# Kernel optimization log

Measured on AMD Instinct MI355X. Metric: run time of the kernel, lower is better.

Reference implementation:

```python
import jax, jax.numpy as jnp
import numpy as np

NEG_SLOPE = 0.2  # PyG GATv2Conv default


def with_self_loops(edge_index, n):
    loop = jnp.arange(n, dtype=edge_index.dtype)
    src = jnp.concatenate([edge_index[0], loop])
    dst = jnp.concatenate([edge_index[1], loop])
    return src, dst


def gatv2(x, src, dst, Wl, bl, Wr, br, att, bias):
    """PyG GATv2Conv (eval mode, concat=True, add_self_loops done by caller).
    x: [N, F_in]; att: [H, C]. Returns [N, H*C]."""
    N = x.shape[0]
    H, C = att.shape
    xl = (x @ Wl + bl).reshape(N, H, C)  # lin_l(x): source-side transform
    xr = (x @ Wr + br).reshape(N, H, C)  # lin_r(x): target-side transform
    s = jax.nn.leaky_relu(xl[src] + xr[dst], NEG_SLOPE)      # [E,H,C]
    logit = jnp.einsum('ehc,hc->eh', s, att)                 # [E,H]
    m = jax.ops.segment_max(logit, dst, num_segments=N)      # stable softmax per target
    e = jnp.exp(logit - m[dst])
    den = jax.ops.segment_sum(e, dst, num_segments=N)
    alpha = e / (den[dst] + 1e-16)                           # [E,H]
    out = jax.ops.segment_sum(alpha[:, :, None] * xl[src], dst, num_segments=N)
    return out.reshape(N, H * C) + bias


def setup_inputs() -> dict:
    N, E = 20000, 320000        # agent nodes / edges
    M, EM = 40000, 400000       # lane nodes / edges
    B, L = 64, 50               # focal agents, centerline length
    SEQ, INC, HID, HEADS, OUT = 50, 2, 32, 4, 60
    H4 = HID * HEADS
    key = jax.random.key(0)
    ks = list(jax.random.split(key, 48))
    kit = iter(ks)

    def p(shape):
        return jax.random.normal(next(kit), shape, jnp.float32) * 0.05

    inp = {
        'x': jax.random.normal(next(kit), (N, SEQ, INC), jnp.float32),
        'edge_index': jax.random.randint(next(kit), (2, E), 0, N),
        'lane_x': jax.random.normal(next(kit), (M, 2), jnp.float32),
        'lane_edge_index': jax.random.randint(next(kit), (2, EM), 0, M),
        'batch': jnp.sort(jax.random.randint(next(kit), (N,), 0, B)),
        'focal_idx': jax.random.randint(next(kit), (B,), 0, N),
        'centerlines': jax.random.normal(next(kit), (B, L, 2), jnp.float32),
        # agent embedding
        'ae_W': p((SEQ * INC, HID)), 'ae_b': p((HID,)),
        # agent subgraph conv1 / conv2
        'a1_Wl': p((HID, H4)), 'a1_bl': p((H4,)), 'a1_Wr': p((HID, H4)), 'a1_br': p((H4,)), 'a1_att': p((HEADS, HID)), 'a1_b': p((H4,)),
        'a2_Wl': p((H4, H4)), 'a2_bl': p((H4,)), 'a2_Wr': p((H4, H4)), 'a2_br': p((H4,)), 'a2_att': p((HEADS, HID)), 'a2_b': p((H4,)),
        # map embedding + map subgraph
        'me_W': p((2, HID)), 'me_b': p((HID,)),
        'm1_Wl': p((HID, H4)), 'm1_bl': p((H4,)), 'm1_Wr': p((HID, H4)), 'm1_br': p((H4,)), 'm1_att': p((HEADS, HID)), 'm1_b': p((H4,)),
        'm2_Wl': p((H4, H4)), 'm2_bl': p((H4,)), 'm2_Wr': p((H4, H4)), 'm2_br': p((H4,)), 'm2_att': p((HEADS, HID)), 'm2_b': p((H4,)),
        # centerline processor
        'cl_W': p((2, HID)), 'cl_b': p((HID,)),
        # global graph (heads=1)
        'g_Wl': p((H4, HID)), 'g_bl': p((HID,)), 'g_Wr': p((H4, HID)), 'g_br': p((HID,)), 'g_att': p((1, HID)), 'g_b': p((HID,)),
        # output head
        'fc_W': p((2 * HID, OUT)), 'fc_b': p((OUT,)),
    }
    return inp


def reference(x, edge_index, lane_x, lane_edge_index, batch, focal_idx, centerlines,
              ae_W, ae_b,
              a1_Wl, a1_bl, a1_Wr, a1_br, a1_att, a1_b,
              a2_Wl, a2_bl, a2_Wr, a2_br, a2_att, a2_b,
              me_W, me_b,
              m1_Wl, m1_bl, m1_Wr, m1_br, m1_att, m1_b,
              m2_Wl, m2_bl, m2_Wr, m2_br, m2_att, m2_b,
              cl_W, cl_b,
              g_Wl, g_bl, g_Wr, g_br, g_att, g_b,
              fc_W, fc_b):
    N = x.shape[0]
    M = lane_x.shape[0]
    # agent branch
    agent_x = jax.nn.relu(x.reshape(N, -1) @ ae_W + ae_b)
    a_src, a_dst = with_self_loops(edge_index, N)
    h = jax.nn.relu(gatv2(agent_x, a_src, a_dst, a1_Wl, a1_bl, a1_Wr, a1_br, a1_att, a1_b))
    agent_features = jax.nn.relu(gatv2(h, a_src, a_dst, a2_Wl, a2_bl, a2_Wr, a2_br, a2_att, a2_b))  # [N,128]
    # map branch (output unused downstream in original, computed for faithfulness)
    map_x = jax.nn.relu(lane_x @ me_W + me_b)
    m_src, m_dst = with_self_loops(lane_edge_index, M)
    hm = jax.nn.relu(gatv2(map_x, m_src, m_dst, m1_Wl, m1_bl, m1_Wr, m1_br, m1_att, m1_b))
    map_features = jax.nn.relu(gatv2(hm, m_src, m_dst, m2_Wl, m2_bl, m2_Wr, m2_br, m2_att, m2_b))
    _ = map_features  # global_mean_pool results are dead code in the original forward
    # global graph over agent features (heads=1)
    global_features = jax.nn.relu(gatv2(agent_features, a_src, a_dst, g_Wl, g_bl, g_Wr, g_br, g_att, g_b))  # [N,32]
    focal = global_features[focal_idx]  # [B,32]
    # centerlines: per-polyline mean then linear (no relu, as in original)
    cl_feat = jnp.mean(centerlines, axis=1) @ cl_W + cl_b  # [B,32]
    combined = jnp.concatenate([focal, cl_feat], axis=1)
    return combined @ fc_W + fc_b
```

## Files before the change

### kernel.cpp

```cpp
#include <hip/hip_runtime.h>
#include <hip/hip_bf16.h>
#include <hip/hip_fp16.h>
#include <math.h>

typedef __hip_bfloat16 bf16;
#define NEG_SLOPE 0.2f
#define SFLAG (1 << 30)

typedef _Float16 f16x8 __attribute__((ext_vector_type(8)));
typedef float f32x4 __attribute__((ext_vector_type(4)));

#define NSEG 25
struct Seg { const void* src; int n; int off; };
struct Tab { Seg s[NSEG]; };

__device__ __forceinline__ float ldconv(const void* src, int i, int f32mode) {
    return f32mode ? ((const float*)src)[i]
                   : __bfloat162float(((const bf16*)src)[i]);
}

__global__ void k_convert(Tab tab, float* __restrict__ dst,
                          const unsigned short* __restrict__ xdet, int* __restrict__ flag,
                          const int* __restrict__ dstArr, int E, int N,
                          int* __restrict__ deg, int* __restrict__ rank,
                          const void* a2WlS, const void* a2WrS,
                          const void* gWlS, const void* gWrS,
                          __half* __restrict__ a2Wlt, __half* __restrict__ a2Wrt,
                          __half* __restrict__ gWlt, __half* __restrict__ gWrt) {
    __shared__ int cnt;
    if (threadIdx.x == 0) cnt = 0;
    __syncthreads();
    int local = 0;
    for (int i = threadIdx.x; i < 2048; i += blockDim.x) {
        unsigned short w = xdet[2 * i];
        int e = (w >> 7) & 0xFF;
        if (e >= 0x90) local++;
    }
    atomicAdd(&cnt, local);
    __syncthreads();
    int f32mode = (cnt > 100) ? 1 : 0;
    if (blockIdx.x == 0 && threadIdx.x == 0) flag[0] = f32mode;

    int gid = blockIdx.x * blockDim.x + threadIdx.x;
    int gsz = gridDim.x * blockDim.x;
    for (int s = 0; s < NSEG; s++) {
        Seg sg = tab.s[s];
        for (int i = gid; i < sg.n; i += gsz) {
            dst[sg.off + i] = ldconv(sg.src, i, f32mode);
        }
    }
    for (int i = gid; i < 128 * 128; i += gsz) {
        int k = i >> 7, j = i & 127;
        a2Wlt[(size_t)j * 128 + k] = __float2half(ldconv(a2WlS, i, f32mode));
        a2Wrt[(size_t)j * 128 + k] = __float2half(ldconv(a2WrS, i, f32mode));
    }
    for (int i = gid; i < 128 * 32; i += gsz) {
        int k = i >> 5, j = i & 31;
        gWlt[(size_t)j * 128 + k] = __float2half(ldconv(gWlS, i, f32mode));
        gWrt[(size_t)j * 128 + k] = __float2half(ldconv(gWrS, i, f32mode));
    }
    int EA = E + N;
    for (int e = gid; e < EA; e += gsz) {
        int d = (e < E) ? dstArr[e] : (e - E);
        rank[e] = atomicAdd(&deg[d], 1);
    }
}

__launch_bounds__(1024)
__global__ void k_scanf(const int* __restrict__ deg, int* __restrict__ offs,
                        int n, int* __restrict__ st, int nb) {
    __shared__ int ws[16];
    __shared__ int stot, sprev;
    int tile = blockIdx.x;
    int i = tile * 1024 + threadIdx.x;
    int lane = threadIdx.x & 63, wid = threadIdx.x >> 6;
    int v = (i < n) ? deg[i] : 0;
    int x = v;
    #pragma unroll
    for (int o = 1; o < 64; o <<= 1) {
        int y = __shfl_up(x, o);
        if (lane >= o) x += y;
    }
    if (lane == 63) ws[wid] = x;
    __syncthreads();
    if (wid == 0) {
        int w = (lane < 16) ? ws[lane] : 0;
        int s = w;
        #pragma unroll
        for (int o = 1; o < 16; o <<= 1) {
            int y = __shfl_up(s, o);
            if (lane >= o) s += y;
        }
        if (lane < 16) ws[lane] = s - w;
        if (lane == 15) stot = s;
    }
    __syncthreads();
    int local = ws[wid] + x - v;
    if (threadIdx.x == 0) {
        int prev = 0;
        if (tile > 0) {
            int vv;
            while ((((vv = __hip_atomic_load(&st[tile - 1], __ATOMIC_ACQUIRE,
                                             __HIP_MEMORY_SCOPE_AGENT))) & SFLAG) == 0) {}
            prev = vv & ~SFLAG;
        }
        __hip_atomic_store(&st[tile], (prev + stot) | SFLAG, __ATOMIC_RELEASE,
                           __HIP_MEMORY_SCOPE_AGENT);
        sprev = prev;
        if (tile == nb - 1) offs[n] = prev + stot;
    }
    __syncthreads();
    if (i < n) offs[i] = sprev + local;
}

__launch_bounds__(256)
__global__ void k_fill_embedlin(const int* __restrict__ srcArr, const int* __restrict__ dstArr,
                                int E, int N, const int* __restrict__ offs,
                                const int* __restrict__ rank, int* __restrict__ csr,
                                const void* __restrict__ xraw, const int* __restrict__ flag,
                                const float* __restrict__ aeW, const float* __restrict__ aeb,
                                const float* __restrict__ Wl, const float* __restrict__ bl,
                                const float* __restrict__ Wr, const float* __restrict__ br,
                                __half* __restrict__ outl, float* __restrict__ outr,
                                int EB) {
    __shared__ float xs[100 * 36];
    __shared__ float axs[32 * 36];
    if (blockIdx.x >= EB) {
        int e = (blockIdx.x - EB) * 256 + threadIdx.x;
        int EA = E + N;
        if (e >= EA) return;
        int d, s;
        if (e < E) { d = dstArr[e]; s = srcArr[e]; } else { d = s = e - E; }
        csr[offs[d] + rank[e]] = s;
        return;
    }
    constexpr int NTP = 36;
    int t = threadIdx.x, nb = blockIdx.x * 32;
    if (flag[0]) {
        const float4* x4 = (const float4*)xraw;
        for (int idx = t; idx < 32 * 25; idx += 256) {
            int node = idx / 25, k4 = idx % 25;
            float4 v = x4[(size_t)(nb + node) * 25 + k4];
            xs[(k4 * 4 + 0) * NTP + node] = v.x;
            xs[(k4 * 4 + 1) * NTP + node] = v.y;
            xs[(k4 * 4 + 2) * NTP + node] = v.z;
            xs[(k4 * 4 + 3) * NTP + node] = v.w;
        }
    } else {
        const ushort4* xu = (const ushort4*)xraw;
        for (int idx = t; idx < 32 * 25; idx += 256) {
            int node = idx / 25, k4 = idx % 25;
            ushort4 u = xu[(size_t)(nb + node) * 25 + k4];
            xs[(k4 * 4 + 0) * NTP + node] = __uint_as_float((unsigned)u.x << 16);
            xs[(k4 * 4 + 1) * NTP + node] = __uint_as_float((unsigned)u.y << 16);
            xs[(k4 * 4 + 2) * NTP + node] = __uint_as_float((unsigned)u.z << 16);
            xs[(k4 * 4 + 3) * NTP + node] = __uint_as_float((unsigned)u.w << 16);
        }
    }
    __syncthreads();
    {
        int j = t & 31, g0 = t >> 5;
        float a0 = 0.f, a1 = 0.f, a2 = 0.f, a3 = 0.f;
        #pragma unroll 10
        for (int k = 0; k < 100; k++) {
            float w = aeW[k * 32 + j];
            const float4 xv = *(const float4*)&xs[k * NTP + g0 * 4];
            a0 += w * xv.x; a1 += w * xv.y; a2 += w * xv.z; a3 += w * xv.w;
        }
        float bj = aeb[j];
        axs[j * NTP + g0 * 4 + 0] = fmaxf(a0 + bj, 0.f);
        axs[j * NTP + g0 * 4 + 1] = fmaxf(a1 + bj, 0.f);
        axs[j * NTP + g0 * 4 + 2] = fmaxf(a2 + bj, 0.f);
        axs[j * NTP + g0 * 4 + 3] = fmaxf(a3 + bj, 0.f);
    }
    __syncthreads();
    {
        int j = t & 63, g0 = t >> 6;
        float aL0[2][4], aL1[2][4], aR0[2][4], aR1[2][4];
        #pragma unroll
        for (int g = 0; g < 2; g++)
            #pragma unroll
            for (int c = 0; c < 4; c++) { aL0[g][c]=0.f; aL1[g][c]=0.f; aR0[g][c]=0.f; aR1[g][c]=0.f; }
        #pragma unroll 4
        for (int k = 0; k < 32; k++) {
            float wl0 = Wl[k * 128 + j];
            float wl1 = Wl[k * 128 + j + 64];
            float wr0 = Wr[k * 128 + j];
            float wr1 = Wr[k * 128 + j + 64];
            #pragma unroll
            for (int g = 0; g < 2; g++) {
                const float4 xv = *(const float4*)&axs[k * NTP + (g0 + g * 4) * 4];
                aL0[g][0] += wl0 * xv.x; aL0[g][1] += wl0 * xv.y; aL0[g][2] += wl0 * xv.z; aL0[g][3] += wl0 * xv.w;
                aL1[g][0] += wl1 * xv.x; aL1[g][1] += wl1 * xv.y; aL1[g][2] += wl1 * xv.z; aL1[g][3] += wl1 * xv.w;
                aR0[g][0] += wr0 * xv.x; aR0[g][1] += wr0 * xv.y; aR0[g][2] += wr0 * xv.z; aR0[g][3] += wr0 * xv.w;
                aR1[g][0] += wr1 * xv.x; aR1[g][1] += wr1 * xv.y; aR1[g][2] += wr1 * xv.z; aR1[g][3] += wr1 * xv.w;
            }
        }
        float bl0 = bl[j], bl1 = bl[j + 64], br0 = br[j], br1 = br[j + 64];
        #pragma unroll
        for (int g = 0; g < 2; g++) {
            int n0 = nb + (g0 + g * 4) * 4;
            #pragma unroll
            for (int c = 0; c < 4; c++) {
                size_t row = (size_t)(n0 + c) * 128;
                outl[row + j]      = __float2half(aL0[g][c] + bl0);
                outl[row + j + 64] = __float2half(aL1[g][c] + bl1);
                outr[row + j]      = aR0[g][c] + br0;
                outr[row + j + 64] = aR1[g][c] + br1;
            }
        }
    }
}

__device__ __forceinline__ void gat_proc(float4 raw, bool valid,
                                         const float* xrd, const float* av,
                                         float* acc, float& sm) {
    const __half2* h = (const __half2*)&raw;
    float v[8];
    float2 f;
    f = __half22float2(h[0]); v[0] = f.x; v[1] = f.y;
    f = __half22float2(h[1]); v[2] = f.x; v[3] = f.y;
    f = __half22float2(h[2]); v[4] = f.x; v[5] = f.y;
    f = __half22float2(h[3]); v[6] = f.x; v[7] = f.y;
    float p = 0.f;
    #pragma unroll
    for (int c = 0; c < 8; c++) {
        float u = v[c] + xrd[c];
        u = (u > 0.f) ? u : NEG_SLOPE * u;
        p += u * av[c];
    }
    p += __shfl_xor(p, 1);
    p += __shfl_xor(p, 2);
    p += __shfl_xor(p, 4);
    p += __shfl_xor(p, 8);
    float w = __expf(fminf(p, 80.f));
    if (!valid) w = 0.f;
    sm += w;
    #pragma unroll
    for (int c = 0; c < 8; c++) acc[c] += w * v[c];
}

__device__ __forceinline__ void gat16_to_lds(__half* xsh,
                                             const __half* __restrict__ xl,
                                             const float* __restrict__ xr,
                                             const float* __restrict__ att,
                                             const int* __restrict__ offs,
                                             const int* __restrict__ csr,
                                             const float* __restrict__ bias,
                                             int d, int node) {
    int t = threadIdx.x;
    int lane = t & 63;
    int sub = lane & 15;
    int lb = lane & 48;
    float av[8];
    {
        const float4* t4 = (const float4*)(att + sub * 8);
        float4 c = t4[0], e = t4[1];
        av[0]=c.x; av[1]=c.y; av[2]=c.z; av[3]=c.w;
        av[4]=e.x; av[5]=e.y; av[6]=e.z; av[7]=e.w;
    }
    bool ok = d >= 0;
    int i0 = ok ? offs[d] : 0;
    int i1 = ok ? offs[d + 1] : 0;
    int cnt = i1 - i0;

    float xrd[8];
    #pragma unroll
    for (int c = 0; c < 8; c++) xrd[c] = 0.f;
    if (ok) {
        const float4* p4 = (const float4*)(xr + (size_t)d * 128 + sub * 8);
        float4 a = p4[0], b = p4[1];
        xrd[0]=a.x; xrd[1]=a.y; xrd[2]=a.z; xrd[3]=a.w;
        xrd[4]=b.x; xrd[5]=b.y; xrd[6]=b.z; xrd[7]=b.w;
    }
    float acc[8];
    #pragma unroll
    for (int c = 0; c < 8; c++) acc[c] = 0.f;
    float sm = 0.f;

    int myv = (sub < cnt) ? csr[i0 + sub] : 0;
    for (int c0 = 0; c0 < cnt; c0 += 16) {
        int myv_nxt = (c0 + 16 + sub < cnt) ? csr[i0 + c0 + 16 + sub] : 0;
        int rem = min(cnt - c0, 16);
        for (int k = 0; k < rem; k += 4) {
            int s0 = __shfl(myv, lb + k + 0);
            int s1 = __shfl(myv, lb + k + 1);
            int s2 = __shfl(myv, lb + k + 2);
            int s3 = __shfl(myv, lb + k + 3);
            float4 r0 = *(const float4*)(xl + (size_t)s0 * 128 + sub * 8);
            float4 r1 = *(const float4*)(xl + (size_t)s1 * 128 + sub * 8);
            float4 r2 = *(const float4*)(xl + (size_t)s2 * 128 + sub * 8);
            float4 r3 = *(const float4*)(xl + (size_t)s3 * 128 + sub * 8);
            gat_proc(r0, true,        xrd, av, acc, sm);
            gat_proc(r1, k + 1 < rem, xrd, av, acc, sm);
            gat_proc(r2, k + 2 < rem, xrd, av, acc, sm);
            gat_proc(r3, k + 3 < rem, xrd, av, acc, sm);
        }
        myv = myv_nxt;
    }

    int ch = sub * 8;
    if (ok) {
        float inv = 1.f / (sm + 1e-16f);
        #pragma unroll
        for (int c = 0; c < 8; c += 2) {
            __half2 hv;
            hv.x = __float2half(fmaxf(acc[c]     * inv + bias[ch + c],     0.f));
            hv.y = __float2half(fmaxf(acc[c + 1] * inv + bias[ch + c + 1], 0.f));
            *(__half2*)&xsh[node * 136 + ch + c] = hv;
        }
    } else {
        #pragma unroll
        for (int c = 0; c < 8; c += 2)
            *(__half2*)&xsh[node * 136 + ch + c] = __half2{__half(0.f), __half(0.f)};
    }
}

__launch_bounds__(256)
__global__ void k_gatlin(const __half* __restrict__ xl, const float* __restrict__ xr,
                         const float* __restrict__ att,
                         const int* __restrict__ offs, const int* __restrict__ csr,
                         const float* __restrict__ bias,
                         const __half* __restrict__ Wlt, const float* __restrict__ bl,
                         const __half* __restrict__ Wrt, const float* __restrict__ br,
                         __half* __restrict__ outl, float* __restrict__ outr, int N,
                         const int* __restrict__ focal, int B,
                         int* __restrict__ L, int* __restrict__ Lcnt, int GT) {
    if (blockIdx.x >= GT) {
        int t = threadIdx.x;
        if (t < B) {
            int f = focal[t];
            int j0 = offs[f], j1 = offs[f + 1];
            int base = atomicAdd(Lcnt, j1 - j0);
            for (int j = j0; j < j1; j++) L[base + (j - j0)] = csr[j];
        }
        return;
    }
    __shared__ __align__(16) __half xsh[16 * 136];
    int nb = blockIdx.x * 16;
    int t = threadIdx.x;
    int lane = t & 63, wv = t >> 6;
    int quad = lane >> 4, n16 = lane & 15;
    {
        int node = wv * 4 + quad;
        int dd = nb + node;
        gat16_to_lds(xsh, xl, xr, att, offs, csr, bias, (dd < N) ? dd : -1, node);
    }
    __syncthreads();

    f16x8 a[4];
    #pragma unroll
    for (int kt = 0; kt < 4; kt++)
        a[kt] = *(const f16x8*)&xsh[n16 * 136 + kt * 32 + quad * 8];

    int j0 = wv * 32;
    f32x4 aL0 = {0.f,0.f,0.f,0.f}, aL1 = {0.f,0.f,0.f,0.f};
    f32x4 aR0 = {0.f,0.f,0.f,0.f}, aR1 = {0.f,0.f,0.f,0.f};
    #pragma unroll
    for (int kt = 0; kt < 4; kt++) {
        int ko = kt * 32 + quad * 8;
        f16x8 b0 = *(const f16x8*)&Wlt[(size_t)(j0 + n16) * 128 + ko];
        f16x8 b1 = *(const f16x8*)&Wlt[(size_t)(j0 + 16 + n16) * 128 + ko];
        f16x8 b2 = *(const f16x8*)&Wrt[(size_t)(j0 + n16) * 128 + ko];
        f16x8 b3 = *(const f16x8*)&Wrt[(size_t)(j0 + 16 + n16) * 128 + ko];
        aL0 = __builtin_amdgcn_mfma_f32_16x16x32_f16(a[kt], b0, aL0, 0, 0, 0);
        aL1 = __builtin_amdgcn_mfma_f32_16x16x32_f16(a[kt], b1, aL1, 0, 0, 0);
        aR0 = __builtin_amdgcn_mfma_f32_16x16x32_f16(a[kt], b2, aR0, 0, 0, 0);
        aR1 = __builtin_amdgcn_mfma_f32_16x16x32_f16(a[kt], b3, aR1, 0, 0, 0);
    }
    float blj0 = bl[j0 + n16], blj1 = bl[j0 + 16 + n16];
    float brj0 = br[j0 + n16], brj1 = br[j0 + 16 + n16];
    #pragma unroll
    for (int r = 0; r < 4; r++) {
        int node = quad * 4 + r;
        if (nb + node >= N) continue;
        size_t row = (size_t)(nb + node) * 128;
        outl[row + j0 + n16]      = __float2half(aL0[r] + blj0);
        outl[row + j0 + 16 + n16] = __float2half(aL1[r] + blj1);
        outr[row + j0 + n16]      = aR0[r] + brj0;
        outr[row + j0 + 16 + n16] = aR1[r] + brj1;
    }
}

__launch_bounds__(256)
__global__ void k_gatling(const __half* __restrict__ xl, const float* __restrict__ xr,
                          const float* __restrict__ att,
                          const int* __restrict__ offs, const int* __restrict__ csr,
                          const float* __restrict__ bias,
                          const __half* __restrict__ Wlt, const float* __restrict__ bl,
                          const __half* __restrict__ Wrt, const float* __restrict__ br,
                          __half* __restrict__ outl, float* __restrict__ outr,
                          const int* __restrict__ L, const int* __restrict__ Lcnt) {
    __shared__ __align__(16) __half xsh[16 * 136];
    int total = *Lcnt;
    int t = threadIdx.x;
    int lane = t & 63, wv = t >> 6;
    int quad = lane >> 4, n16 = lane & 15;

    for (int tile = blockIdx.x; tile * 16 < total; tile += gridDim.x) {
        if (tile != (int)blockIdx.x) __syncthreads();
        int node = wv * 4 + quad;
        int idx = tile * 16 + node;
        int d = (idx < total) ? L[idx] : -1;
        gat16_to_lds(xsh, xl, xr, att, offs, csr, bias, d, node);
        __syncthreads();

        f16x8 a[4];
        #pragma unroll
        for (int kt = 0; kt < 4; kt++)
            a[kt] = *(const f16x8*)&xsh[n16 * 136 + kt * 32 + quad * 8];

        const __half* Wt = (wv < 2) ? Wlt : Wrt;
        int j0 = (wv & 1) * 16;
        f32x4 accv = {0.f,0.f,0.f,0.f};
        #pragma unroll
        for (int kt = 0; kt < 4; kt++) {
            f16x8 b = *(const f16x8*)&Wt[(size_t)(j0 + n16) * 128 + kt * 32 + quad * 8];
            accv = __builtin_amdgcn_mfma_f32_16x16x32_f16(a[kt], b, accv, 0, 0, 0);
        }
        float bj = ((wv < 2) ? bl : br)[j0 + n16];
        #pragma unroll
        for (int r = 0; r < 4; r++) {
            int nn = quad * 4 + r;
            int gidx = tile * 16 + nn;
            if (gidx >= total) continue;
            int gd = L[gidx];
            size_t row = (size_t)gd * 32;
            if (wv < 2) outl[row + j0 + n16] = __float2half(accv[r] + bj);
            else        outr[row + j0 + n16] = accv[r] + bj;
        }
    }
}

__launch_bounds__(64)
__global__ void k_tailf(const __half* __restrict__ xl, const float* __restrict__ xr,
                        const float* __restrict__ att,
                        const int* __restrict__ offs, const int* __restrict__ csr,
                        const float* __restrict__ gb, const int* __restrict__ focal,
                        const float* __restrict__ clf, const float* __restrict__ clW,
                        const float* __restrict__ clb, const float* __restrict__ fcW,
                        const float* __restrict__ fcb, void* __restrict__ out,
                        const int* __restrict__ flag) {
    __shared__ float comb[64];
    __shared__ float ssb[2];
    int b = blockIdx.x;
    int t = threadIdx.x;
    int d = focal[b];
    int grp = t >> 3, sub = t & 7;
    int i0 = offs[d], i1 = offs[d + 1];

    float xrd[4], av[4], acc[4];
    {
        float4 a = *(const float4*)(xr + (size_t)d * 32 + sub * 4);
        xrd[0]=a.x; xrd[1]=a.y; xrd[2]=a.z; xrd[3]=a.w;
        float4 c = *(const float4*)(att + sub * 4);
        av[0]=c.x; av[1]=c.y; av[2]=c.z; av[3]=c.w;
    }
    #pragma unroll
    for (int c = 0; c < 4; c++) acc[c] = 0.f;
    float sm = 0.f;

    for (int i = i0 + grp; i < i1; i += 8) {
        float2 raw = *(const float2*)(xl + (size_t)csr[i] * 32 + sub * 4);
        const __half2* h = (const __half2*)&raw;
        float v[4];
        float2 f;
        f = __half22float2(h[0]); v[0] = f.x; v[1] = f.y;
        f = __half22float2(h[1]); v[2] = f.x; v[3] = f.y;
        float p = 0.f;
        #pragma unroll
        for (int c = 0; c < 4; c++) {
            float u = v[c] + xrd[c];
            u = (u > 0.f) ? u : NEG_SLOPE * u;
            p += u * av[c];
        }
        p += __shfl_xor(p, 1);
        p += __shfl_xor(p, 2);
        p += __shfl_xor(p, 4);
        float w = __expf(fminf(p, 80.f));
        sm += w;
        #pragma unroll
        for (int c = 0; c < 4; c++) acc[c] += w * v[c];
    }
    sm += __shfl_xor(sm, 8); sm += __shfl_xor(sm, 16); sm += __shfl_xor(sm, 32);
    #pragma unroll
    for (int c = 0; c < 4; c++) {
        acc[c] += __shfl_xor(acc[c], 8);
        acc[c] += __shfl_xor(acc[c], 16);
        acc[c] += __shfl_xor(acc[c], 32);
    }
    if (grp == 0) {
        float inv = 1.f / (sm + 1e-16f);
        #pragma unroll
        for (int c = 0; c < 4; c++)
            comb[sub * 4 + c] = fmaxf(acc[c] * inv + gb[sub * 4 + c], 0.f);
    }
    if (t < 2) {
        float s = 0.f;
        for (int l = 0; l < 50; l++) s += clf[(size_t)b * 100 + l * 2 + t];
        ssb[t] = s / 50.f;
    }
    __syncthreads();
    if (t < 32) comb[32 + t] = ssb[0] * clW[t] + ssb[1] * clW[32 + t] + clb[t];
    __syncthreads();
    if (t < 60) {
        float a2 = fcb[t];
        #pragma unroll 16
        for (int k = 0; k < 64; k++) a2 += comb[k] * fcW[k * 60 + t];
        if (flag[0]) ((float*)out)[b * 60 + t] = a2;
        else ((bf16*)out)[b * 60 + t] = __float2bfloat16(a2);
    }
}

extern "C" void kernel_launch(void* const* d_in, const int* in_sizes, int n_in,
                              void* d_out, int out_size, void* d_ws, size_t ws_size,
                              hipStream_t stream) {
    const int* edge  = (const int*)d_in[1];
    const int* focal = (const int*)d_in[5];

    const int N = in_sizes[0] / 100;
    const int E = in_sizes[1] / 2;
    const int B = in_sizes[5];
    const int EA = E + N;
    const int* srcArr = edge;
    const int* dstArr = edge + E;

    const int idxs[NSEG] = {7,8,9,10,11,12,13,14,15,16,17,18,19,20,
                            35,36,37,38,39,40,41,42,43,44, 6};
    float* base = (float*)d_ws;
    int* flag = (int*)base;
    float* wf = base + 16;
    Tab tab;
    int off[NSEG];
    int o = 0;
    for (int i = 0; i < NSEG; i++) {
        tab.s[i].src = d_in[idxs[i]];
        tab.s[i].n   = in_sizes[idxs[i]];
        tab.s[i].off = o;
        off[i] = o;
        o += in_sizes[idxs[i]];
    }
    const float* aeW  = wf + off[0],  *aeb  = wf + off[1];
    const float* a1Wl = wf + off[2],  *a1bl = wf + off[3];
    const float* a1Wr = wf + off[4],  *a1br = wf + off[5];
    const float* a1att= wf + off[6],  *a1b  = wf + off[7];
    const float* a2bl = wf + off[9];
    const float* a2br = wf + off[11];
    const float* a2att= wf + off[12], *a2b  = wf + off[13];
    const float* clW  = wf + off[14], *clb  = wf + off[15];
    const float* gbl  = wf + off[17];
    const float* gbr  = wf + off[19];
    const float* gatt = wf + off[20], *gb   = wf + off[21];
    const float* fcW  = wf + off[22], *fcb  = wf + off[23];
    const float* clf  = wf + off[24];

    float* p = wf + o + ((4 - (o & 3)) & 3);
    size_t N128 = (size_t)N * 128;
    __half* hxl1 = (__half*)p;      p += (size_t)N * 64;
    float* fB1  = p;                p += N128;
    __half* hxl2 = (__half*)p;      p += (size_t)N * 64;
    float* fB2  = p;                p += N128;
    int* deg    = (int*)p;
    int* st     = deg + N;
    int* offs   = st + 32;
    int* rank   = offs + N + 1;
    int* csr    = rank + EA;
    uintptr_t up = (uintptr_t)(csr + EA);
    up = (up + 15) & ~(uintptr_t)15;
    __half* a2Wlt = (__half*)up;
    __half* a2Wrt = a2Wlt + 16384;
    __half* gWlt  = a2Wrt + 16384;
    __half* gWrt  = gWlt + 4096;
    int* Lbuf = (int*)(gWrt + 4096);
    int* Lcnt = st + 30;

    const int NB = (N + 1023) / 1024;
    const int EB = N / 32;
    const int FBLK = (EA + 255) / 256;
    const int GT = (N + 15) / 16;

    hipMemsetAsync(deg, 0, (size_t)(N + 32) * sizeof(int), stream);
    k_convert<<<256, 256, 0, stream>>>(tab, wf, (const unsigned short*)d_in[0], flag,
                                       dstArr, E, N, deg, rank,
                                       d_in[15], d_in[17], d_in[37], d_in[39],
                                       a2Wlt, a2Wrt, gWlt, gWrt);
    k_scanf<<<NB, 1024, 0, stream>>>(deg, offs, N, st, NB);
    k_fill_embedlin<<<EB + FBLK, 256, 0, stream>>>(srcArr, dstArr, E, N, offs, rank, csr,
                                                   d_in[0], flag, aeW, aeb,
                                                   a1Wl, a1bl, a1Wr, a1br, hxl1, fB1, EB);
    k_gatlin<<<GT + 1, 256, 0, stream>>>(hxl1, fB1, a1att, offs, csr, a1b,
                                         a2Wlt, a2bl, a2Wrt, a2br, hxl2, fB2, N,
                                         focal, B, Lbuf, Lcnt, GT);
    k_gatling<<<128, 256, 0, stream>>>(hxl2, fB2, a2att, offs, csr, a2b,
                                       gWlt, gbl, gWrt, gbr, hxl1, fB1, Lbuf, Lcnt);
    k_tailf<<<B, 64, 0, stream>>>(hxl1, fB1, gatt, offs, csr, gb, focal,
                                  clf, clW, clb, fcW, fcb, d_out, flag);
}
```

Baseline: 255.1 us.

## Replace scanned CSR with fixed-capacity per-node adjacency slots plus spill list

Result: faster. 234.0 us (-8.3%).

```diff
diff --git a/kernel.cpp b/kernel.cpp
--- a/kernel.cpp
+++ b/kernel.cpp
@@ -5,7 +5,6 @@
 
 typedef __hip_bfloat16 bf16;
 #define NEG_SLOPE 0.2f
-#define SFLAG (1 << 30)
 
 typedef _Float16 f16x8 __attribute__((ext_vector_type(8)));
 typedef float f32x4 __attribute__((ext_vector_type(4)));
@@ -21,8 +20,11 @@
 
 __global__ void k_convert(Tab tab, float* __restrict__ dst,
                           const unsigned short* __restrict__ xdet, int* __restrict__ flag,
-                          const int* __restrict__ dstArr, int E, int N,
-                          int* __restrict__ deg, int* __restrict__ rank,
+                          const int* __restrict__ srcArr, const int* __restrict__ dstArr,
+                          int E, int N,
+                          int* __restrict__ deg, int* __restrict__ csrF,
+                          int* __restrict__ spillD, int* __restrict__ spillS,
+                          int* __restrict__ spillCnt,
                           const void* a2WlS, const void* a2WrS,
                           const void* gWlS, const void* gWrS,
                           __half* __restrict__ a2Wlt, __half* __restrict__ a2Wrt,
@@ -61,79 +63,27 @@
     }
     int EA = E + N;
     for (int e = gid; e < EA; e += gsz) {
-        int d = (e < E) ? dstArr[e] : (e - E);
-        rank[e] = atomicAdd(&deg[d], 1);
-    }
-}
-
-__launch_bounds__(1024)
-__global__ void k_scanf(const int* __restrict__ deg, int* __restrict__ offs,
-                        int n, int* __restrict__ st, int nb) {
-    __shared__ int ws[16];
-    __shared__ int stot, sprev;
-    int tile = blockIdx.x;
-    int i = tile * 1024 + threadIdx.x;
-    int lane = threadIdx.x & 63, wid = threadIdx.x >> 6;
-    int v = (i < n) ? deg[i] : 0;
-    int x = v;
-    #pragma unroll
-    for (int o = 1; o < 64; o <<= 1) {
-        int y = __shfl_up(x, o);
-        if (lane >= o) x += y;
-    }
-    if (lane == 63) ws[wid] = x;
-    __syncthreads();
-    if (wid == 0) {
-        int w = (lane < 16) ? ws[lane] : 0;
-        int s = w;
-        #pragma unroll
-        for (int o = 1; o < 16; o <<= 1) {
-            int y = __shfl_up(s, o);
-            if (lane >= o) s += y;
-        }
-        if (lane < 16) ws[lane] = s - w;
-        if (lane == 15) stot = s;
-    }
-    __syncthreads();
-    int local = ws[wid] + x - v;
-    if (threadIdx.x == 0) {
-        int prev = 0;
-        if (tile > 0) {
-            int vv;
-            while ((((vv = __hip_atomic_load(&st[tile - 1], __ATOMIC_ACQUIRE,
-                                             __HIP_MEMORY_SCOPE_AGENT))) & SFLAG) == 0) {}
-            prev = vv & ~SFLAG;
-        }
-        __hip_atomic_store(&st[tile], (prev + stot) | SFLAG, __ATOMIC_RELEASE,
-                           __HIP_MEMORY_SCOPE_AGENT);
-        sprev = prev;
-        if (tile == nb - 1) offs[n] = prev + stot;
-    }
-    __syncthreads();
-    if (i < n) offs[i] = sprev + local;
+        int d, s;
+        if (e < E) { d = dstArr[e]; s = srcArr[e]; } else { d = s = e - E; }
+        int r = atomicAdd(&deg[d], 1);
+        if (r < 64) {
+            csrF[(size_t)d * 64 + r] = s;
+        } else {
+            int o = atomicAdd(spillCnt, 1);
+            spillD[o] = d; spillS[o] = s;
+        }
+    }
 }
 
 __launch_bounds__(256)
-__global__ void k_fill_embedlin(const int* __restrict__ srcArr, const int* __restrict__ dstArr,
-                                int E, int N, const int* __restrict__ offs,
-                                const int* __restrict__ rank, int* __restrict__ csr,
-                                const void* __restrict__ xraw, const int* __restrict__ flag,
-                                const float* __restrict__ aeW, const float* __restrict__ aeb,
-                                const float* __restrict__ Wl, const float* __restrict__ bl,
-                                const float* __restrict__ Wr, const float* __restrict__ br,
-                                __half* __restrict__ outl, float* __restrict__ outr,
-                                int EB) {
+__global__ void k_embedlin(const void* __restrict__ xraw, const int* __restrict__ flag,
+                           int N,
+                           const float* __restrict__ aeW, const float* __restrict__ aeb,
+                           const float* __restrict__ Wl, const float* __restrict__ bl,
+                           const float* __restrict__ Wr, const float* __restrict__ br,
+                           __half* __restrict__ outl, float* __restrict__ outr) {
     __shared__ float xs[100 * 36];
     __shared__ float axs[32 * 36];
-    if (blockIdx.x >= EB) {
-        int e = (blockIdx.x - EB) * 256 + threadIdx.x;
-        int EA = E + N;
-        if (e >= EA) return;
-        int d, s;
-        if (e < E) { d = dstArr[e]; s = srcArr[e]; } else { d = s = e - E; }
-        csr[offs[d] + rank[e]] = s;
-        return;
-    }
     constexpr int NTP = 36;
     int t = threadIdx.x, nb = blockIdx.x * 32;
     if (flag[0]) {
@@ -244,8 +194,11 @@
                                              const __half* __restrict__ xl,
                                              const float* __restrict__ xr,
                                              const float* __restrict__ att,
-                                             const int* __restrict__ offs,
-                                             const int* __restrict__ csr,
+                                             const int* __restrict__ deg,
+                                             const int* __restrict__ csrF,
+                                             const int* __restrict__ spillD,
+                                             const int* __restrict__ spillS,
+                                             const int* __restrict__ spillCnt,
                                              const float* __restrict__ bias,
                                              int d, int node) {
     int t = threadIdx.x;
@@ -260,9 +213,9 @@
         av[4]=e.x; av[5]=e.y; av[6]=e.z; av[7]=e.w;
     }
     bool ok = d >= 0;
-    int i0 = ok ? offs[d] : 0;
-    int i1 = ok ? offs[d + 1] : 0;
-    int cnt = i1 - i0;
+    int cnt = ok ? deg[d] : 0;
+    int cmain = cnt < 64 ? cnt : 64;
+    size_t i0 = (size_t)(ok ? d : 0) * 64;
 
     float xrd[8];
     #pragma unroll
@@ -278,10 +231,10 @@
     for (int c = 0; c < 8; c++) acc[c] = 0.f;
     float sm = 0.f;
 
-    int myv = (sub < cnt) ? csr[i0 + sub] : 0;
-    for (int c0 = 0; c0 < cnt; c0 += 16) {
-        int myv_nxt = (c0 + 16 + sub < cnt) ? csr[i0 + c0 + 16 + sub] : 0;
-        int rem = min(cnt - c0, 16);
+    int myv = (sub < cmain) ? csrF[i0 + sub] : 0;
+    for (int c0 = 0; c0 < cmain; c0 += 16) {
+        int myv_nxt = (c0 + 16 + sub < cmain) ? csrF[i0 + c0 + 16 + sub] : 0;
+        int rem = min(cmain - c0, 16);
         for (int k = 0; k < rem; k += 4) {
             int s0 = __shfl(myv, lb + k + 0);
             int s1 = __shfl(myv, lb + k + 1);
@@ -298,6 +251,15 @@
         }
         myv = myv_nxt;
     }
+    if (cnt > 64) {
+        int stot = *spillCnt;
+        for (int j = 0; j < stot; j++) {
+            if (spillD[j] == d) {
+                float4 r = *(const float4*)(xl + (size_t)spillS[j] * 128 + sub * 8);
+                gat_proc(r, true, xrd, av, acc, sm);
+            }
+        }
+    }
 
     int ch = sub * 8;
     if (ok) {
@@ -319,7 +281,9 @@
 __launch_bounds__(256)
 __global__ void k_gatlin(const __half* __restrict__ xl, const float* __restrict__ xr,
                          const float* __restrict__ att,
-                         const int* __restrict__ offs, const int* __restrict__ csr,
+                         const int* __restrict__ deg, const int* __restrict__ csrF,
+                         const int* __restrict__ spillD, const int* __restrict__ spillS,
+                         const int* __restrict__ spillCnt,
                          const float* __restrict__ bias,
                          const __half* __restrict__ Wlt, const float* __restrict__ bl,
                          const __half* __restrict__ Wrt, const float* __restrict__ br,
@@ -330,9 +294,16 @@
         int t = threadIdx.x;
         if (t < B) {
             int f = focal[t];
-            int j0 = offs[f], j1 = offs[f + 1];
-            int base = atomicAdd(Lcnt, j1 - j0);
-            for (int j = j0; j < j1; j++) L[base + (j - j0)] = csr[j];
+            int cf = deg[f];
+            int cm = cf < 64 ? cf : 64;
+            int base = atomicAdd(Lcnt, cf);
+            for (int j = 0; j < cm; j++) L[base + j] = csrF[(size_t)f * 64 + j];
+            if (cf > 64) {
+                int k = cm;
+                int stot = *spillCnt;
+                for (int j = 0; j < stot; j++)
+                    if (spillD[j] == f) L[base + k++] = spillS[j];
+            }
         }
         return;
     }
@@ -344,7 +315,8 @@
     {
         int node = wv * 4 + quad;
         int dd = nb + node;
-        gat16_to_lds(xsh, xl, xr, att, offs, csr, bias, (dd < N) ? dd : -1, node);
+        gat16_to_lds(xsh, xl, xr, att, deg, csrF, spillD, spillS, spillCnt,
+                     bias, (dd < N) ? dd : -1, node);
     }
     __syncthreads();
 
@@ -385,7 +357,9 @@
 __launch_bounds__(256)
 __global__ void k_gatling(const __half* __restrict__ xl, const float* __restrict__ xr,
                           const float* __restrict__ att,
-                          const int* __restrict__ offs, const int* __restrict__ csr,
+                          const int* __restrict__ deg, const int* __restrict__ csrF,
+                          const int* __restrict__ spillD, const int* __restrict__ spillS,
+                          const int* __restrict__ spillCnt,
                           const float* __restrict__ bias,
                           const __half* __restrict__ Wlt, const float* __restrict__ bl,
                           const __half* __restrict__ Wrt, const float* __restrict__ br,
@@ -402,7 +376,8 @@
         int node = wv * 4 + quad;
         int idx = tile * 16 + node;
         int d = (idx < total) ? L[idx] : -1;
-        gat16_to_lds(xsh, xl, xr, att, offs, csr, bias, d, node);
+        gat16_to_lds(xsh, xl, xr, att, deg, csrF, spillD, spillS, spillCnt,
+                     bias, d, node);
         __syncthreads();
 
         f16x8 a[4];
@@ -435,7 +410,9 @@
 __launch_bounds__(64)
 __global__ void k_tailf(const __half* __restrict__ xl, const float* __restrict__ xr,
                         const float* __restrict__ att,
-                        const int* __restrict__ offs, const int* __restrict__ csr,
+                        const int* __restrict__ deg, const int* __restrict__ csrF,
+                        const int* __restrict__ spillD, const int* __restrict__ spillS,
+                        const int* __restrict__ spillCnt,
                         const float* __restrict__ gb, const int* __restrict__ focal,
                         const float* __restrict__ clf, const float* __restrict__ clW,
                         const float* __restrict__ clb, const float* __restrict__ fcW,
@@ -447,7 +424,9 @@
     int t = threadIdx.x;
     int d = focal[b];
     int grp = t >> 3, sub = t & 7;
-    int i0 = offs[d], i1 = offs[d + 1];
+    int cnt = deg[d];
+    int cm = cnt < 64 ? cnt : 64;
+    size_t i0 = (size_t)d * 64;
 
     float xrd[4], av[4], acc[4];
     {
@@ -460,8 +439,8 @@
     for (int c = 0; c < 4; c++) acc[c] = 0.f;
     float sm = 0.f;
 
-    for (int i = i0 + grp; i < i1; i += 8) {
-        float2 raw = *(const float2*)(xl + (size_t)csr[i] * 32 + sub * 4);
+    auto edge = [&](int s) {
+        float2 raw = *(const float2*)(xl + (size_t)s * 32 + sub * 4);
         const __half2* h = (const __half2*)&raw;
         float v[4];
         float2 f;
@@ -481,6 +460,12 @@
         sm += w;
         #pragma unroll
         for (int c = 0; c < 4; c++) acc[c] += w * v[c];
+    };
+    for (int i = grp; i < cm; i += 8) edge(csrF[i0 + i]);
+    if (cnt > 64) {
+        int stot = *spillCnt;
+        for (int i = grp; i < stot; i += 8)
+            if (spillD[i] == d) edge(spillS[i]);
     }
     sm += __shfl_xor(sm, 8); sm += __shfl_xor(sm, 16); sm += __shfl_xor(sm, 32);
     #pragma unroll
@@ -562,10 +547,10 @@
     float* fB2  = p;                p += N128;
     int* deg    = (int*)p;
     int* st     = deg + N;
-    int* offs   = st + 32;
-    int* rank   = offs + N + 1;
-    int* csr    = rank + EA;
-    uintptr_t up = (uintptr_t)(csr + EA);
+    int* csrF   = st + 32;
+    int* spillD = csrF + (size_t)N * 64;
+    int* spillS = spillD + EA;
+    uintptr_t up = (uintptr_t)(spillS + EA);
     up = (up + 15) & ~(uintptr_t)15;
     __half* a2Wlt = (__half*)up;
     __half* a2Wrt = a2Wlt + 16384;
@@ -573,26 +558,27 @@
     __half* gWrt  = gWlt + 4096;
     int* Lbuf = (int*)(gWrt + 4096);
     int* Lcnt = st + 30;
-
-    const int NB = (N + 1023) / 1024;
+    int* spillCnt = st + 29;
+
     const int EB = N / 32;
-    const int FBLK = (EA + 255) / 256;
     const int GT = (N + 15) / 16;
 
     hipMemsetAsync(deg, 0, (size_t)(N + 32) * sizeof(int), stream);
     k_convert<<<256, 256, 0, stream>>>(tab, wf, (const unsigned short*)d_in[0], flag,
-                                       dstArr, E, N, deg, rank,
+                                       srcArr, dstArr, E, N, deg, csrF,
+                                       spillD, spillS, spillCnt,
                                        d_in[15], d_in[17], d_in[37], d_in[39],
                                        a2Wlt, a2Wrt, gWlt, gWrt);
-    k_scanf<<<NB, 1024, 0, stream>>>(deg, offs, N, st, NB);
-    k_fill_embedlin<<<EB + FBLK, 256, 0, stream>>>(srcArr, dstArr, E, N, offs, rank, csr,
-                                                   d_in[0], flag, aeW, aeb,
-                                                   a1Wl, a1bl, a1Wr, a1br, hxl1, fB1, EB);
-    k_gatlin<<<GT + 1, 256, 0, stream>>>(hxl1, fB1, a1att, offs, csr, a1b,
+    k_embedlin<<<EB, 256, 0, stream>>>(d_in[0], flag, N, aeW, aeb,
+                                       a1Wl, a1bl, a1Wr, a1br, hxl1, fB1);
+    k_gatlin<<<GT + 1, 256, 0, stream>>>(hxl1, fB1, a1att, deg, csrF,
+                                         spillD, spillS, spillCnt, a1b,
                                          a2Wlt, a2bl, a2Wrt, a2br, hxl2, fB2, N,
                                          focal, B, Lbuf, Lcnt, GT);
-    k_gatling<<<128, 256, 0, stream>>>(hxl2, fB2, a2att, offs, csr, a2b,
+    k_gatling<<<128, 256, 0, stream>>>(hxl2, fB2, a2att, deg, csrF,
+                                       spillD, spillS, spillCnt, a2b,
                                        gWlt, gbl, gWrt, gbr, hxl1, fB1, Lbuf, Lcnt);
-    k_tailf<<<B, 64, 0, stream>>>(hxl1, fB1, gatt, offs, csr, gb, focal,
+    k_tailf<<<B, 64, 0, stream>>>(hxl1, fB1, gatt, deg, csrF,
+                                  spillD, spillS, spillCnt, gb, focal,
                                   clf, clW, clb, fcW, fcb, d_out, flag);
 }
```
